# Performance work log

Hardware: AMD Instinct MI355X
Metric: run time of the kernel (lower is better)

Reference implementation:

```python
import jax, jax.numpy as jnp
import numpy as np

RH, RW = 4, 4

def window_sum(x, rh, rw):
    # cumsum along H (axis 2)
    cum_h = jnp.cumsum(x, axis=2)
    wh = 2 * rh + 1
    top = cum_h[:, :, rh:wh, :]
    midh = cum_h[:, :, wh:, :] - cum_h[:, :, :-wh, :]
    bot = cum_h[:, :, -1:, :] - cum_h[:, :, -wh:-rh - 1, :]
    out = jnp.concatenate([top, midh, bot], axis=2)
    # cumsum along W (axis 3)
    cum_w = jnp.cumsum(out, axis=3)
    ww = 2 * rw + 1
    left = cum_w[:, :, :, rw:ww]
    midw = cum_w[:, :, :, ww:] - cum_w[:, :, :, :-ww]
    right = cum_w[:, :, :, -1:] - cum_w[:, :, :, -ww:-rw - 1]
    return jnp.concatenate([left, midw, right], axis=3)


def setup_inputs() -> dict:
    key = jax.random.key(0)
    x = jax.random.normal(key, (16, 3, 1024, 1024), dtype=jnp.float32)
    return {"x": x}


def reference(x):
    win_sum = window_sum(x, RH, RW)
    count = window_sum(jnp.ones_like(x), RH, RW)
    return win_sum / count
```

## Files before the change

### kernel.cpp

```cpp
#include <hip/hip_runtime.h>

#define HH 1024
#define WW 1024
#define BH 64
#define RAD 4
#define NSTRIP (HH / BH)

struct HS { float h0, h1, h2, h3; };

__device__ __forceinline__ HS hcompute(float4 a, float4 b, float4 d) {
    HS h;
    h.h0 = ((a.x + a.y) + (a.z + a.w)) + ((b.x + b.y) + (b.z + b.w)) + d.x;
    h.h1 = h.h0 - a.x + d.y;
    h.h2 = h.h1 - a.y + d.z;
    h.h3 = h.h2 - a.z + d.w;
    return h;
}

#define LOADROW(pa, pb, pd, rowptr) do {                                   \
    pb = *(const float4*)((rowptr) + c);                                   \
    pa = first ? z4 : *(const float4*)((rowptr) + c - 4);                  \
    pd = last  ? z4 : *(const float4*)((rowptr) + c + 4);                  \
} while (0)

#define PSTEP(J, PX) do {                                                  \
    HS h = hcompute(pa##PX, pb##PX, pd##PX);                               \
    LOADROW(pa##PX, pb##PX, pd##PX, rowp); rowp += WW;                     \
    vs0 += h.h0 - ring[J].h0;                                              \
    vs1 += h.h1 - ring[J].h1;                                              \
    vs2 += h.h2 - ring[J].h2;                                              \
    vs3 += h.h3 - ring[J].h3;                                              \
    ring[J] = h;                                                           \
    *(float4*)(op + c) = make_float4(vs0 * w0, vs1 * w1, vs2 * w2, vs3 * w3); \
    op += WW;                                                              \
} while (0)

#define GSTEP(J) do {                                                      \
    int rl = r + RAD;                                                      \
    HS h;                                                                  \
    if (rl < HH) {                                                         \
        float4 a, b, d;                                                    \
        LOADROW(a, b, d, xin + (size_t)rl * WW);                           \
        h = hcompute(a, b, d);                                             \
    } else { h.h0 = h.h1 = h.h2 = h.h3 = 0.f; }                            \
    vs0 += h.h0 - ring[J].h0;                                              \
    vs1 += h.h1 - ring[J].h1;                                              \
    vs2 += h.h2 - ring[J].h2;                                              \
    vs3 += h.h3 - ring[J].h3;                                              \
    ring[J] = h;                                                           \
    int lo = r - RAD; if (lo < 0) lo = 0;                                  \
    int hi = r + RAD; if (hi > HH - 1) hi = HH - 1;                        \
    float ich = 1.0f / (float)(hi - lo + 1);                               \
    *(float4*)(o + (size_t)r * WW + c) =                                   \
        make_float4(vs0 * ich * sw[0], vs1 * ich * sw[1],                  \
                    vs2 * ich * sw[2], vs3 * ich * sw[3]);                 \
    ++r;                                                                   \
} while (0)

__global__ __launch_bounds__(256, 3)
void box_kernel(const float* __restrict__ x, float* __restrict__ out) {
    const int tid = threadIdx.x;

    const int lin  = blockIdx.x + NSTRIP * blockIdx.y;
    const int nblk = NSTRIP * gridDim.y;
    const int cpx  = nblk >> 3;
    const int swz  = (lin & 7) * cpx + (lin >> 3);
    const int strip = swz & (NSTRIP - 1);
    const int img   = swz / NSTRIP;

    const int r0 = strip * BH;
    const int c  = tid * 4;
    const bool first = (tid == 0);
    const bool last  = (tid == 255);
    const float4 z4 = make_float4(0.f, 0.f, 0.f, 0.f);

    const float* __restrict__ xin = x + (size_t)img * (HH * WW);
    float* __restrict__ o = out + (size_t)img * (HH * WW);

    float sw[4];
#pragma unroll
    for (int j = 0; j < 4; ++j) {
        int cc = c + j;
        int lo = cc - RAD < 0 ? 0 : cc - RAD;
        int hi = cc + RAD > WW - 1 ? WW - 1 : cc + RAD;
        sw[j] = 1.0f / (float)(hi - lo + 1);
    }

    HS ring[9];
    float vs0 = 0.f, vs1 = 0.f, vs2 = 0.f, vs3 = 0.f;
#pragma unroll
    for (int k = 0; k < 9; ++k) {
        int rr = r0 - RAD - 1 + k;
        HS h;
        if (rr >= 0) {
            float4 a, b, d;
            LOADROW(a, b, d, xin + (size_t)rr * WW);
            h = hcompute(a, b, d);
        } else { h.h0 = h.h1 = h.h2 = h.h3 = 0.f; }
        ring[k] = h;
        vs0 += h.h0; vs1 += h.h1; vs2 += h.h2; vs3 += h.h3;
    }

    const bool interior = (r0 >= RAD) && (r0 + BH + RAD <= HH);

    if (interior) {
        const float w0 = sw[0] * (1.0f / 9.0f);
        const float w1 = sw[1] * (1.0f / 9.0f);
        const float w2 = sw[2] * (1.0f / 9.0f);
        const float w3 = sw[3] * (1.0f / 9.0f);

        float4 pa0, pb0, pd0, pa1, pb1, pd1, pa2, pb2, pd2;
        const float* rowp = xin + (size_t)(r0 + RAD) * WW;
        LOADROW(pa0, pb0, pd0, rowp); rowp += WW;
        LOADROW(pa1, pb1, pd1, rowp); rowp += WW;
        LOADROW(pa2, pb2, pd2, rowp); rowp += WW;

        float* op = o + (size_t)r0 * WW;
#pragma unroll 1
        for (int chunk = 0; chunk < 7; ++chunk) {
            PSTEP(0, 0); PSTEP(1, 1); PSTEP(2, 2);
            PSTEP(3, 0); PSTEP(4, 1); PSTEP(5, 2);
            PSTEP(6, 0); PSTEP(7, 1); PSTEP(8, 2);
        }
        PSTEP(0, 0);
    } else {
        int r = r0;
#pragma unroll 1
        for (int chunk = 0; chunk < 7; ++chunk) {
            GSTEP(0); GSTEP(1); GSTEP(2); GSTEP(3); GSTEP(4);
            GSTEP(5); GSTEP(6); GSTEP(7); GSTEP(8);
        }
        GSTEP(0);
    }
}

extern "C" void kernel_launch(void* const* d_in, const int* in_sizes, int n_in,
                              void* d_out, int out_size, void* d_ws, size_t ws_size,
                              hipStream_t stream) {
    const float* x = (const float*)d_in[0];
    float* out = (float*)d_out;
    int n_images = in_sizes[0] / (HH * WW);
    dim3 grid(NSTRIP, n_images);
    dim3 block(256);
    box_kernel<<<grid, block, 0, stream>>>(x, out);
}
```

Before: 387.8 us.

## Share neighbor columns via cross-lane permute, move ring buffer to LDS, deepen prefetch

Each row is now fetched with a single float4 load per thread. The left and right neighbor float4s come from adjacent lanes through ds_bpermute, and only the wave-edge lanes issue an extra load. The 9-entry horizontal-sum ring buffer moves from registers to shared memory, which frees registers for a 6-deep row prefetch instead of 3-deep. The cost is eight LDS permutes plus an LDS read and write per row step, which adds LDS traffic and latency in exchange for fewer redundant global loads.

```diff
diff --git a/kernel.cpp b/kernel.cpp
--- a/kernel.cpp
+++ b/kernel.cpp
@@ -17,48 +17,86 @@
     return h;
 }
 
+__device__ __forceinline__ float shfl1(int addr, float v) {
+    return __int_as_float(__builtin_amdgcn_ds_bpermute(addr, __float_as_int(v)));
+}
+
 #define LOADROW(pa, pb, pd, rowptr) do {                                   \
     pb = *(const float4*)((rowptr) + c);                                   \
     pa = first ? z4 : *(const float4*)((rowptr) + c - 4);                  \
     pd = last  ? z4 : *(const float4*)((rowptr) + c + 4);                  \
 } while (0)
 
-#define PSTEP(J, PX) do {                                                  \
-    HS h = hcompute(pa##PX, pb##PX, pd##PX);                               \
-    LOADROW(pa##PX, pb##PX, pd##PX, rowp); rowp += WW;                     \
-    vs0 += h.h0 - ring[J].h0;                                              \
-    vs1 += h.h1 - ring[J].h1;                                              \
-    vs2 += h.h2 - ring[J].h2;                                              \
-    vs3 += h.h3 - ring[J].h3;                                              \
-    ring[J] = h;                                                           \
-    *(float4*)(op + c) = make_float4(vs0 * w0, vs1 * w1, vs2 * w2, vs3 * w3); \
+#define PFETCH(X) do {                                                     \
+    pb##X = *(const float4*)(rowp + c);                                    \
+    if (eAny) pe##X = *(const float4*)(rowp + eoff);                       \
+    rowp += WW;                                                            \
+} while (0)
+
+#define PFETCHB(X) do {                                                    \
+    const float* rp = xin + (size_t)(pr < HH ? pr : (HH - 1)) * WW;        \
+    pb##X = *(const float4*)(rp + c);                                      \
+    if (eAny) pe##X = *(const float4*)(rp + eoff);                         \
+    ++pr;                                                                  \
+} while (0)
+
+#define BUILD_AD()                                                         \
+    float4 a, d;                                                           \
+    a.x = shfl1(addrU, b.x); a.y = shfl1(addrU, b.y);                      \
+    a.z = shfl1(addrU, b.z); a.w = shfl1(addrU, b.w);                      \
+    d.x = shfl1(addrD, b.x); d.y = shfl1(addrD, b.y);                      \
+    d.z = shfl1(addrD, b.z); d.w = shfl1(addrD, b.w);                      \
+    if (lane == 0)  a = first ? z4 : pev;                                  \
+    if (lane == 63) d = last  ? z4 : pev;
+
+#define ISTEP(J, PX) do {                                                  \
+    float4 b   = pb##PX;                                                   \
+    float4 pev = pe##PX;                                                   \
+    PFETCH(PX);                                  \
+    BUILD_AD();                                                            \
+    HS h = hcompute(a, b, d);                                              \
+    float4 hold = hring[J][tid];                                           \
+    vs0 += h.h0 - hold.x; vs1 += h.h1 - hold.y;                            \
+    vs2 += h.h2 - hold.z; vs3 += h.h3 - hold.w;                            \
+    hring[J][tid] = make_float4(h.h0, h.h1, h.h2, h.h3);                   \
+    *(float4*)op = make_float4(vs0 * w0, vs1 * w1, vs2 * w2, vs3 * w3);    \
     op += WW;                                                              \
 } while (0)
 
-#define GSTEP(J) do {                                                      \
-    int rl = r + RAD;                                                      \
-    HS h;                                                                  \
-    if (rl < HH) {                                                         \
-        float4 a, b, d;                                                    \
-        LOADROW(a, b, d, xin + (size_t)rl * WW);                           \
-        h = hcompute(a, b, d);                                             \
-    } else { h.h0 = h.h1 = h.h2 = h.h3 = 0.f; }                            \
-    vs0 += h.h0 - ring[J].h0;                                              \
-    vs1 += h.h1 - ring[J].h1;                                              \
-    vs2 += h.h2 - ring[J].h2;                                              \
-    vs3 += h.h3 - ring[J].h3;                                              \
-    ring[J] = h;                                                           \
-    int lo = r - RAD; if (lo < 0) lo = 0;                                  \
-    int hi = r + RAD; if (hi > HH - 1) hi = HH - 1;                        \
+#define BSTEP(J, PX) do {                                                  \
+    float4 b   = pb##PX;                                                   \
+    float4 pev = pe##PX;                                                   \
+    PFETCHB(PX);                                                           \
+    BUILD_AD();                                                            \
+    HS h = hcompute(a, b, d);                                              \
+    bool valid = (r + RAD) < HH;                                           \
+    h.h0 = valid ? h.h0 : 0.f; h.h1 = valid ? h.h1 : 0.f;                  \
+    h.h2 = valid ? h.h2 : 0.f; h.h3 = valid ? h.h3 : 0.f;                  \
+    float4 hold = hring[J][tid];                                           \
+    vs0 += h.h0 - hold.x; vs1 += h.h1 - hold.y;                            \
+    vs2 += h.h2 - hold.z; vs3 += h.h3 - hold.w;                            \
+    hring[J][tid] = make_float4(h.h0, h.h1, h.h2, h.h3);                   \
+    int lo = r - RAD; lo = lo < 0 ? 0 : lo;                                \
+    int hi = r + RAD; hi = hi > HH - 1 ? HH - 1 : hi;                      \
     float ich = 1.0f / (float)(hi - lo + 1);                               \
-    *(float4*)(o + (size_t)r * WW + c) =                                   \
-        make_float4(vs0 * ich * sw[0], vs1 * ich * sw[1],                  \
-                    vs2 * ich * sw[2], vs3 * ich * sw[3]);                 \
-    ++r;                                                                   \
+    *(float4*)op = make_float4(vs0 * ich * sw[0], vs1 * ich * sw[1],       \
+                               vs2 * ich * sw[2], vs3 * ich * sw[3]);      \
+    op += WW; ++r;                                                         \
 } while (0)
 
-__global__ __launch_bounds__(256, 3)
+#define CHUNK18(STEP)                                                      \
+    STEP(0,0); STEP(1,1); STEP(2,2); STEP(3,3); STEP(4,4); STEP(5,5);      \
+    STEP(6,0); STEP(7,1); STEP(8,2); STEP(0,3); STEP(1,4); STEP(2,5);      \
+    STEP(3,0); STEP(4,1); STEP(5,2); STEP(6,3); STEP(7,4); STEP(8,5);
+#define TAIL10(STEP)                                                       \
+    STEP(0,0); STEP(1,1); STEP(2,2); STEP(3,3); STEP(4,4);                 \
+    STEP(5,5); STEP(6,0); STEP(7,1); STEP(8,2); STEP(0,3);
+
+__global__ __launch_bounds__(256)
+__attribute__((amdgpu_waves_per_eu(3, 3)))
 void box_kernel(const float* __restrict__ x, float* __restrict__ out) {
+    __shared__ float4 hring[9][256];
+
     const int tid = threadIdx.x;
 
     const int lin  = blockIdx.x + NSTRIP * blockIdx.y;
@@ -70,9 +108,18 @@
 
     const int r0 = strip * BH;
     const int c  = tid * 4;
+    const int lane = tid & 63;
     const bool first = (tid == 0);
     const bool last  = (tid == 255);
     const float4 z4 = make_float4(0.f, 0.f, 0.f, 0.f);
+
+    const int addrU = ((lane - 1) & 63) << 2;
+    const int addrD = ((lane + 1) & 63) << 2;
+
+    const bool eLo  = (lane == 0)  && !first;
+    const bool eHi  = (lane == 63) && !last;
+    const bool eAny = eLo || eHi;
+    const int  eoff = eLo ? (c - 4) : (c + 4);
 
     const float* __restrict__ xin = x + (size_t)img * (HH * WW);
     float* __restrict__ o = out + (size_t)img * (HH * WW);
@@ -86,7 +133,6 @@
         sw[j] = 1.0f / (float)(hi - lo + 1);
     }
 
-    HS ring[9];
     float vs0 = 0.f, vs1 = 0.f, vs2 = 0.f, vs3 = 0.f;
 #pragma unroll
     for (int k = 0; k < 9; ++k) {
@@ -97,11 +143,15 @@
             LOADROW(a, b, d, xin + (size_t)rr * WW);
             h = hcompute(a, b, d);
         } else { h.h0 = h.h1 = h.h2 = h.h3 = 0.f; }
-        ring[k] = h;
+        hring[k][tid] = make_float4(h.h0, h.h1, h.h2, h.h3);
         vs0 += h.h0; vs1 += h.h1; vs2 += h.h2; vs3 += h.h3;
     }
 
     const bool interior = (r0 >= RAD) && (r0 + BH + RAD <= HH);
+
+    float4 pb0, pb1, pb2, pb3, pb4, pb5;
+    float4 pe0 = z4, pe1 = z4, pe2 = z4, pe3 = z4, pe4 = z4, pe5 = z4;
+    float* op = o + (size_t)r0 * WW + c;
 
     if (interior) {
         const float w0 = sw[0] * (1.0f / 9.0f);
@@ -109,28 +159,24 @@
         const float w2 = sw[2] * (1.0f / 9.0f);
         const float w3 = sw[3] * (1.0f / 9.0f);
 
-        float4 pa0, pb0, pd0, pa1, pb1, pd1, pa2, pb2, pd2;
         const float* rowp = xin + (size_t)(r0 + RAD) * WW;
-        LOADROW(pa0, pb0, pd0, rowp); rowp += WW;
-        LOADROW(pa1, pb1, pd1, rowp); rowp += WW;
-        LOADROW(pa2, pb2, pd2, rowp); rowp += WW;
+        PFETCH(0); PFETCH(1); PFETCH(2); PFETCH(3); PFETCH(4); PFETCH(5);
 
-        float* op = o + (size_t)r0 * WW;
 #pragma unroll 1
-        for (int chunk = 0; chunk < 7; ++chunk) {
-            PSTEP(0, 0); PSTEP(1, 1); PSTEP(2, 2);
-            PSTEP(3, 0); PSTEP(4, 1); PSTEP(5, 2);
-            PSTEP(6, 0); PSTEP(7, 1); PSTEP(8, 2);
+        for (int chunk = 0; chunk < 3; ++chunk) {
+            CHUNK18(ISTEP)
         }
-        PSTEP(0, 0);
+        TAIL10(ISTEP)
     } else {
         int r = r0;
+        int pr = r0 + RAD;
+        PFETCHB(0); PFETCHB(1); PFETCHB(2); PFETCHB(3); PFETCHB(4); PFETCHB(5);
+
 #pragma unroll 1
-        for (int chunk = 0; chunk < 7; ++chunk) {
-            GSTEP(0); GSTEP(1); GSTEP(2); GSTEP(3); GSTEP(4);
-            GSTEP(5); GSTEP(6); GSTEP(7); GSTEP(8);
+        for (int chunk = 0; chunk < 3; ++chunk) {
+            CHUNK18(BSTEP)
         }
-        GSTEP(0);
+        TAIL10(BSTEP)
     }
 }
 
```

Measured after the change: 360.8 us. 1.07x faster.

## Move row-sum ring to LDS and double-buffer four-row load groups

Applied to the files above, without the earlier changes.

Moves the 9-entry horizontal-sum ring buffer from registers into shared memory, which frees VGPRs. The freed registers hold two groups of four input rows, so each group is loaded while the previous group is consumed. This raises memory-level parallelism per thread. The boundary path now clamps row indices instead of branching and zeroes rows past the end. In exchange it adds 36KB of LDS per block, extra LDS traffic per row, and a fixed waves-per-EU attribute.

```diff
diff --git a/kernel.cpp b/kernel.cpp
--- a/kernel.cpp
+++ b/kernel.cpp
@@ -23,42 +23,59 @@
     pd = last  ? z4 : *(const float4*)((rowptr) + c + 4);                  \
 } while (0)
 
-#define PSTEP(J, PX) do {                                                  \
-    HS h = hcompute(pa##PX, pb##PX, pd##PX);                               \
-    LOADROW(pa##PX, pb##PX, pd##PX, rowp); rowp += WW;                     \
-    vs0 += h.h0 - ring[J].h0;                                              \
-    vs1 += h.h1 - ring[J].h1;                                              \
-    vs2 += h.h2 - ring[J].h2;                                              \
-    vs3 += h.h3 - ring[J].h3;                                              \
-    ring[J] = h;                                                           \
-    *(float4*)(op + c) = make_float4(vs0 * w0, vs1 * w1, vs2 * w2, vs3 * w3); \
+#define LOADG(S) do {                                                      \
+    LOADROW(a##S##0, b##S##0, d##S##0, rowp); rowp += WW;                  \
+    LOADROW(a##S##1, b##S##1, d##S##1, rowp); rowp += WW;                  \
+    LOADROW(a##S##2, b##S##2, d##S##2, rowp); rowp += WW;                  \
+    LOADROW(a##S##3, b##S##3, d##S##3, rowp); rowp += WW;                  \
+} while (0)
+
+#define LOADGB(S) do {                                                     \
+    const float* rp;                                                       \
+    rp = xin + (size_t)(prow < HH ? prow : (HH - 1)) * WW; ++prow;         \
+    LOADROW(a##S##0, b##S##0, d##S##0, rp);                                \
+    rp = xin + (size_t)(prow < HH ? prow : (HH - 1)) * WW; ++prow;         \
+    LOADROW(a##S##1, b##S##1, d##S##1, rp);                                \
+    rp = xin + (size_t)(prow < HH ? prow : (HH - 1)) * WW; ++prow;         \
+    LOADROW(a##S##2, b##S##2, d##S##2, rp);                                \
+    rp = xin + (size_t)(prow < HH ? prow : (HH - 1)) * WW; ++prow;         \
+    LOADROW(a##S##3, b##S##3, d##S##3, rp);                                \
+} while (0)
+
+#define CONS1(S, K) do {                                                   \
+    HS h = hcompute(a##S##K, b##S##K, d##S##K);                            \
+    float4 hold = hring[slot][tid];                                        \
+    vs0 += h.h0 - hold.x; vs1 += h.h1 - hold.y;                            \
+    vs2 += h.h2 - hold.z; vs3 += h.h3 - hold.w;                            \
+    hring[slot][tid] = make_float4(h.h0, h.h1, h.h2, h.h3);                \
+    slot = (slot == 8) ? 0 : slot + 1;                                     \
+    *(float4*)op = make_float4(vs0 * w0, vs1 * w1, vs2 * w2, vs3 * w3);    \
     op += WW;                                                              \
 } while (0)
+#define CONSG(S) do { CONS1(S,0); CONS1(S,1); CONS1(S,2); CONS1(S,3); } while (0)
 
-#define GSTEP(J) do {                                                      \
-    int rl = r + RAD;                                                      \
-    HS h;                                                                  \
-    if (rl < HH) {                                                         \
-        float4 a, b, d;                                                    \
-        LOADROW(a, b, d, xin + (size_t)rl * WW);                           \
-        h = hcompute(a, b, d);                                             \
-    } else { h.h0 = h.h1 = h.h2 = h.h3 = 0.f; }                            \
-    vs0 += h.h0 - ring[J].h0;                                              \
-    vs1 += h.h1 - ring[J].h1;                                              \
-    vs2 += h.h2 - ring[J].h2;                                              \
-    vs3 += h.h3 - ring[J].h3;                                              \
-    ring[J] = h;                                                           \
-    int lo = r - RAD; if (lo < 0) lo = 0;                                  \
-    int hi = r + RAD; if (hi > HH - 1) hi = HH - 1;                        \
+#define CONS1B(S, K) do {                                                  \
+    HS h = hcompute(a##S##K, b##S##K, d##S##K);                            \
+    if (r + RAD >= HH) { h.h0 = 0.f; h.h1 = 0.f; h.h2 = 0.f; h.h3 = 0.f; } \
+    float4 hold = hring[slot][tid];                                        \
+    vs0 += h.h0 - hold.x; vs1 += h.h1 - hold.y;                            \
+    vs2 += h.h2 - hold.z; vs3 += h.h3 - hold.w;                            \
+    hring[slot][tid] = make_float4(h.h0, h.h1, h.h2, h.h3);                \
+    slot = (slot == 8) ? 0 : slot + 1;                                     \
+    int lo = r - RAD; lo = lo < 0 ? 0 : lo;                                \
+    int hi = r + RAD; hi = hi > HH - 1 ? HH - 1 : hi;                      \
     float ich = 1.0f / (float)(hi - lo + 1);                               \
-    *(float4*)(o + (size_t)r * WW + c) =                                   \
-        make_float4(vs0 * ich * sw[0], vs1 * ich * sw[1],                  \
-                    vs2 * ich * sw[2], vs3 * ich * sw[3]);                 \
-    ++r;                                                                   \
+    *(float4*)op = make_float4(vs0 * ich * sw[0], vs1 * ich * sw[1],       \
+                               vs2 * ich * sw[2], vs3 * ich * sw[3]);      \
+    op += WW; ++r;                                                         \
 } while (0)
+#define CONSGB(S) do { CONS1B(S,0); CONS1B(S,1); CONS1B(S,2); CONS1B(S,3); } while (0)
 
-__global__ __launch_bounds__(256, 3)
+__global__ __launch_bounds__(256)
+__attribute__((amdgpu_waves_per_eu(3, 3)))
 void box_kernel(const float* __restrict__ x, float* __restrict__ out) {
+    __shared__ float4 hring[9][256];
+
     const int tid = threadIdx.x;
 
     const int lin  = blockIdx.x + NSTRIP * blockIdx.y;
@@ -86,7 +103,6 @@
         sw[j] = 1.0f / (float)(hi - lo + 1);
     }
 
-    HS ring[9];
     float vs0 = 0.f, vs1 = 0.f, vs2 = 0.f, vs3 = 0.f;
 #pragma unroll
     for (int k = 0; k < 9; ++k) {
@@ -97,11 +113,17 @@
             LOADROW(a, b, d, xin + (size_t)rr * WW);
             h = hcompute(a, b, d);
         } else { h.h0 = h.h1 = h.h2 = h.h3 = 0.f; }
-        ring[k] = h;
+        hring[k][tid] = make_float4(h.h0, h.h1, h.h2, h.h3);
         vs0 += h.h0; vs1 += h.h1; vs2 += h.h2; vs3 += h.h3;
     }
 
     const bool interior = (r0 >= RAD) && (r0 + BH + RAD <= HH);
+
+    float4 aA0, bA0, dA0, aA1, bA1, dA1, aA2, bA2, dA2, aA3, bA3, dA3;
+    float4 aB0, bB0, dB0, aB1, bB1, dB1, aB2, bB2, dB2, aB3, bB3, dB3;
+
+    float* op = o + (size_t)r0 * WW + c;
+    int slot = 0;
 
     if (interior) {
         const float w0 = sw[0] * (1.0f / 9.0f);
@@ -109,28 +131,26 @@
         const float w2 = sw[2] * (1.0f / 9.0f);
         const float w3 = sw[3] * (1.0f / 9.0f);
 
-        float4 pa0, pb0, pd0, pa1, pb1, pd1, pa2, pb2, pd2;
         const float* rowp = xin + (size_t)(r0 + RAD) * WW;
-        LOADROW(pa0, pb0, pd0, rowp); rowp += WW;
-        LOADROW(pa1, pb1, pd1, rowp); rowp += WW;
-        LOADROW(pa2, pb2, pd2, rowp); rowp += WW;
-
-        float* op = o + (size_t)r0 * WW;
+        LOADG(A);
 #pragma unroll 1
-        for (int chunk = 0; chunk < 7; ++chunk) {
-            PSTEP(0, 0); PSTEP(1, 1); PSTEP(2, 2);
-            PSTEP(3, 0); PSTEP(4, 1); PSTEP(5, 2);
-            PSTEP(6, 0); PSTEP(7, 1); PSTEP(8, 2);
+        for (int it = 0; it < 7; ++it) {
+            LOADG(B); CONSG(A);
+            LOADG(A); CONSG(B);
         }
-        PSTEP(0, 0);
+        LOADG(B); CONSG(A);
+        CONSG(B);
     } else {
+        int prow = r0 + RAD;
         int r = r0;
+        LOADGB(A);
 #pragma unroll 1
-        for (int chunk = 0; chunk < 7; ++chunk) {
-            GSTEP(0); GSTEP(1); GSTEP(2); GSTEP(3); GSTEP(4);
-            GSTEP(5); GSTEP(6); GSTEP(7); GSTEP(8);
+        for (int it = 0; it < 7; ++it) {
+            LOADGB(B); CONSGB(A);
+            LOADGB(A); CONSGB(B);
         }
-        GSTEP(0);
+        LOADGB(B); CONSGB(A);
+        CONSGB(B);
     }
 }
 
```

Result: faster. 379.5 us (-2.1%).
